# Kernel tuning notes

Measured on AMD Instinct MI355X. Metric: run time of the kernel, lower is better.

The kernel has to match this reference:

```python
import jax, jax.numpy as jnp
import numpy as np

SCALE = 2
KSIZE = 3
EPS = 0.2  # damping constant in 1/(grad^2 + 0.2)


def _unfold_patches(x, k):
    """x: [B, C, H, W] -> [B, C, k*k, H, W], zero-padded, row-major window order
    (matches torch.nn.functional.unfold channel ordering)."""
    B, C, H, W = x.shape
    p = k // 2
    xp = jnp.pad(x, ((0, 0), (0, 0), (p, p), (p, p)))
    return jnp.stack(
        [xp[:, :, i:i + H, j:j + W] for i in range(k) for j in range(k)], axis=2
    )


def setup_inputs() -> dict:
    key = jax.random.key(0)
    x = jax.random.normal(key, (4, 128, 128, 128), dtype=jnp.float32)
    return {"x": x}


def reference(x):
    B, C, H, W = x.shape
    k, s = KSIZE, SCALE
    k2 = k * k

    # channel-mean map [B, 1, H, W]
    mean = jnp.mean(x, axis=1, keepdims=True)

    # local gradients of the mean map: unfold(mean) - mean  -> [B, k2, H, W]
    grad = _unfold_patches(mean, k)[:, 0] - mean
    grad = 1.0 / (grad * grad + EPS)

    # nearest-neighbor upsample by s (F.interpolate default mode='nearest')
    up = jnp.repeat(jnp.repeat(grad, s, axis=2), s, axis=3)  # [B, k2, Hs, Ws]
    kernels = jax.nn.softmax(up, axis=1)

    # CARAFE content-aware reassembly (group=1):
    # output pixel (i, j) gathers the kxk neighborhood of source pixel
    # (i//s, j//s) of x and reduces it with kernels[:, :, i, j].
    patches = _unfold_patches(x, k)                 # [B, C, k2, H, W]
    Kr = kernels.reshape(B, k2, H, s, W, s)         # split upsampled grid
    out = jnp.einsum('bkhpwq,bckhw->bchpwq', Kr, patches)
    return out.reshape(B, C, H * s, W * s)
```

## Files before the change

kernel.cpp:

```cpp
#include <hip/hip_runtime.h>

#define NB 4
#define NC 128
#define NH 128
#define NW 128
#define EPSV 0.2f
#define TH 2

typedef float v2f __attribute__((ext_vector_type(2)));

__global__ __launch_bounds__(256) void mean_kernel(const float* __restrict__ x,
                                                   float* __restrict__ mean) {
    const int tid = threadIdx.x;
    const int pos = tid & 31;
    const int cg  = tid >> 5;
    const int gpos = blockIdx.x * 32 + pos;
    const int b    = gpos >> 12;
    const int pos4 = gpos & 4095;

    const float4* x4 = (const float4*)x;
    float4 acc = make_float4(0.f, 0.f, 0.f, 0.f);
    const int cbase = (b * NC + cg * 16) * (NH * NW / 4) + pos4;
    #pragma unroll
    for (int cc = 0; cc < 16; ++cc) {
        float4 v = x4[cbase + cc * (NH * NW / 4)];
        acc.x += v.x; acc.y += v.y; acc.z += v.z; acc.w += v.w;
    }

    __shared__ float4 red[256];
    red[tid] = acc;
    __syncthreads();
    if (tid < 32) {
        float4 s = red[tid];
        #pragma unroll
        for (int g = 1; g < 8; ++g) {
            float4 v = red[tid + 32 * g];
            s.x += v.x; s.y += v.y; s.z += v.z; s.w += v.w;
        }
        const float inv = 1.0f / NC;
        s.x *= inv; s.y *= inv; s.z *= inv; s.w *= inv;
        ((float4*)mean)[blockIdx.x * 32 + tid] = s;
    }
}

__global__ __launch_bounds__(256) void carafe_kernel(const float* __restrict__ x,
                                                     const float* __restrict__ mean,
                                                     float* __restrict__ out) {
    const int nx = gridDim.x;
    const int chunk = nx >> 3;
    const int bid = blockIdx.x;
    const int swz = (bid & 7) * chunk + (bid >> 3);

    const int b  = swz >> 6;
    const int h0 = (swz & 63) * TH;
    const int cq = blockIdx.y;

    __shared__ float wgt[TH][9][NW];

    const int tid = threadIdx.x;
    const float* mb = mean + (size_t)b * NH * NW;

    {
        const int r = tid >> 7;
        const int w = tid & 127;
        const int h = h0 + r;
        const float mc = mb[h * NW + w];
        float v[9];
        float vmax = -1e30f;
        #pragma unroll
        for (int ky = -1; ky <= 1; ++ky) {
            #pragma unroll
            for (int kx = -1; kx <= 1; ++kx) {
                const int hh = h + ky, ww = w + kx;
                const float mp = (hh >= 0 && hh < NH && ww >= 0 && ww < NW)
                                     ? mb[hh * NW + ww] : 0.0f;
                const float g = mp - mc;
                const float val = 1.0f / (g * g + EPSV);
                v[(ky + 1) * 3 + (kx + 1)] = val;
                vmax = fmaxf(vmax, val);
            }
        }
        float sum = 0.f;
        #pragma unroll
        for (int k = 0; k < 9; ++k) { v[k] = __expf(v[k] - vmax); sum += v[k]; }
        const float rs = 1.0f / sum;
        #pragma unroll
        for (int k = 0; k < 9; ++k) wgt[r][k][w] = v[k] * rs;
    }
    __syncthreads();

    const int w     = tid & (NW - 1);
    const int chalf = tid >> 7;

    float wk0[9], wk1[9];
    #pragma unroll
    for (int k = 0; k < 9; ++k) { wk0[k] = wgt[0][k][w]; wk1[k] = wgt[1][k][w]; }

    const bool hm = (h0 > 0);
    const bool hp = (h0 + TH < NH);
    const bool wm = (w > 0), wp = (w < NW - 1);

    for (int it = 0; it < 16; ++it) {
        const int c = cq * 32 + it * 2 + chalf;
        const float* xb = x + ((size_t)(b * NC + c)) * (NH * NW);

        float a[4][3];
        #pragma unroll
        for (int rr = 0; rr < 4; ++rr) {
            const int hh = h0 - 1 + rr;
            const bool hv = (rr == 0) ? hm : ((rr == 3) ? hp : true);
            const float* row = xb + hh * NW;
            a[rr][0] = (hv && wm) ? row[w - 1] : 0.f;
            a[rr][1] = hv ? row[w] : 0.f;
            a[rr][2] = (hv && wp) ? row[w + 1] : 0.f;
        }

        float v0 = 0.f, v1 = 0.f;
        #pragma unroll
        for (int ky = 0; ky < 3; ++ky) {
            #pragma unroll
            for (int kx = 0; kx < 3; ++kx) {
                v0 += wk0[ky * 3 + kx] * a[ky][kx];
                v1 += wk1[ky * 3 + kx] * a[ky + 1][kx];
            }
        }

        float* outc = out + ((size_t)(b * NC + c)) * (NH * 2) * (NW * 2);
        float* r0 = outc + (size_t)(2 * h0) * (NW * 2) + 2 * w;
        const v2f p0 = {v0, v0};
        const v2f p1 = {v1, v1};
        __builtin_nontemporal_store(p0, (v2f*)(r0));
        __builtin_nontemporal_store(p0, (v2f*)(r0 + (NW * 2)));
        __builtin_nontemporal_store(p1, (v2f*)(r0 + 2 * (NW * 2)));
        __builtin_nontemporal_store(p1, (v2f*)(r0 + 3 * (NW * 2)));
    }
}

extern "C" void kernel_launch(void* const* d_in, const int* in_sizes, int n_in,
                              void* d_out, int out_size, void* d_ws, size_t ws_size,
                              hipStream_t stream) {
    const float* x = (const float*)d_in[0];
    float* out = (float*)d_out;
    float* mean = (float*)d_ws;

    mean_kernel<<<dim3(512), dim3(256), 0, stream>>>(x, mean);
    carafe_kernel<<<dim3(NB * NH / TH, 4), dim3(256), 0, stream>>>(x, mean, out);
}
```

Baseline: 39.57 us.

## Fuse channel-mean into CARAFE kernel and widen per-thread output to float4

Removes the separate mean kernel: each block recomputes the channel mean for its two rows plus halo rows directly from x into shared memory, then builds the softmax weights and does the reassembly in one launch. The grid drops the channel-quarter dimension and uses 512-thread blocks, each thread handling 16 channels and two adjacent output columns so it emits 16-byte stores. This saves a launch and the mean round trip through memory, but each block now redundantly reads 4 rows across all 128 channels. Block count also falls to 256, which may limit latency hiding.

```diff
diff --git a/kernel.cpp b/kernel.cpp
--- a/kernel.cpp
+++ b/kernel.cpp
@@ -7,76 +7,51 @@
 #define EPSV 0.2f
 #define TH 2
 
-typedef float v2f __attribute__((ext_vector_type(2)));
+typedef float v4f __attribute__((ext_vector_type(4)));
 
-__global__ __launch_bounds__(256) void mean_kernel(const float* __restrict__ x,
-                                                   float* __restrict__ mean) {
-    const int tid = threadIdx.x;
-    const int pos = tid & 31;
-    const int cg  = tid >> 5;
-    const int gpos = blockIdx.x * 32 + pos;
-    const int b    = gpos >> 12;
-    const int pos4 = gpos & 4095;
-
-    const float4* x4 = (const float4*)x;
-    float4 acc = make_float4(0.f, 0.f, 0.f, 0.f);
-    const int cbase = (b * NC + cg * 16) * (NH * NW / 4) + pos4;
-    #pragma unroll
-    for (int cc = 0; cc < 16; ++cc) {
-        float4 v = x4[cbase + cc * (NH * NW / 4)];
-        acc.x += v.x; acc.y += v.y; acc.z += v.z; acc.w += v.w;
-    }
-
-    __shared__ float4 red[256];
-    red[tid] = acc;
-    __syncthreads();
-    if (tid < 32) {
-        float4 s = red[tid];
-        #pragma unroll
-        for (int g = 1; g < 8; ++g) {
-            float4 v = red[tid + 32 * g];
-            s.x += v.x; s.y += v.y; s.z += v.z; s.w += v.w;
-        }
-        const float inv = 1.0f / NC;
-        s.x *= inv; s.y *= inv; s.z *= inv; s.w *= inv;
-        ((float4*)mean)[blockIdx.x * 32 + tid] = s;
-    }
-}
-
-__global__ __launch_bounds__(256) void carafe_kernel(const float* __restrict__ x,
-                                                     const float* __restrict__ mean,
-                                                     float* __restrict__ out) {
-    const int nx = gridDim.x;
-    const int chunk = nx >> 3;
+__global__ __launch_bounds__(512) void fused_carafe(const float* __restrict__ x,
+                                                    float* __restrict__ out) {
+    const int chunk = gridDim.x >> 3;
     const int bid = blockIdx.x;
     const int swz = (bid & 7) * chunk + (bid >> 3);
-
     const int b  = swz >> 6;
     const int h0 = (swz & 63) * TH;
-    const int cq = blockIdx.y;
 
+    __shared__ float mrow[4][NW];
     __shared__ float wgt[TH][9][NW];
 
     const int tid = threadIdx.x;
-    const float* mb = mean + (size_t)b * NH * NW;
 
     {
         const int r = tid >> 7;
         const int w = tid & 127;
-        const int h = h0 + r;
-        const float mc = mb[h * NW + w];
+        const int hh = h0 - 1 + r;
+        float s = 0.f;
+        if (hh >= 0 && hh < NH) {
+            const float* px = x + ((size_t)b * NC * NH + hh) * NW + w;
+            #pragma unroll 16
+            for (int c = 0; c < NC; ++c)
+                s += px[(size_t)c * NH * NW];
+        }
+        mrow[r][w] = s * (1.0f / NC);
+    }
+    __syncthreads();
+
+    if (tid < 256) {
+        const int r = tid >> 7;
+        const int w = tid & 127;
+        const float mc = mrow[r + 1][w];
         float v[9];
         float vmax = -1e30f;
         #pragma unroll
-        for (int ky = -1; ky <= 1; ++ky) {
+        for (int ky = 0; ky < 3; ++ky) {
             #pragma unroll
             for (int kx = -1; kx <= 1; ++kx) {
-                const int hh = h + ky, ww = w + kx;
-                const float mp = (hh >= 0 && hh < NH && ww >= 0 && ww < NW)
-                                     ? mb[hh * NW + ww] : 0.0f;
+                const int ww = w + kx;
+                const float mp = (ww >= 0 && ww < NW) ? mrow[r + ky][ww] : 0.f;
                 const float g = mp - mc;
                 const float val = 1.0f / (g * g + EPSV);
-                v[(ky + 1) * 3 + (kx + 1)] = val;
+                v[ky * 3 + kx + 1] = val;
                 vmax = fmaxf(vmax, val);
             }
         }
@@ -89,50 +64,57 @@
     }
     __syncthreads();
 
-    const int w     = tid & (NW - 1);
-    const int chalf = tid >> 7;
+    const int wp = tid & 63;
+    const int cg = tid >> 6;
+    const int wa = 2 * wp;
 
-    float wk0[9], wk1[9];
+    float wA0[9], wB0[9], wA1[9], wB1[9];
     #pragma unroll
-    for (int k = 0; k < 9; ++k) { wk0[k] = wgt[0][k][w]; wk1[k] = wgt[1][k][w]; }
+    for (int k = 0; k < 9; ++k) {
+        wA0[k] = wgt[0][k][wa];  wB0[k] = wgt[0][k][wa + 1];
+        wA1[k] = wgt[1][k][wa];  wB1[k] = wgt[1][k][wa + 1];
+    }
 
-    const bool hm = (h0 > 0);
-    const bool hp = (h0 + TH < NH);
-    const bool wm = (w > 0), wp = (w < NW - 1);
+    const bool rv0 = (h0 > 0), rv3 = (h0 + 2 < NH);
+    const bool tv0 = (wp > 0), tv3 = (wp < 63);
 
-    for (int it = 0; it < 16; ++it) {
-        const int c = cq * 32 + it * 2 + chalf;
-        const float* xb = x + ((size_t)(b * NC + c)) * (NH * NW);
+    #pragma unroll 2
+    for (int i = 0; i < 16; ++i) {
+        const int c = cg * 16 + i;
+        const float* xc = x + ((size_t)(b * NC + c)) * (NH * NW);
 
-        float a[4][3];
+        float a[4][4];
         #pragma unroll
         for (int rr = 0; rr < 4; ++rr) {
             const int hh = h0 - 1 + rr;
-            const bool hv = (rr == 0) ? hm : ((rr == 3) ? hp : true);
-            const float* row = xb + hh * NW;
-            a[rr][0] = (hv && wm) ? row[w - 1] : 0.f;
-            a[rr][1] = hv ? row[w] : 0.f;
-            a[rr][2] = (hv && wp) ? row[w + 1] : 0.f;
+            const bool rv = (rr == 0) ? rv0 : ((rr == 3) ? rv3 : true);
+            const float* row = xc + hh * NW + wa;
+            a[rr][0] = (rv && tv0) ? row[-1] : 0.f;
+            a[rr][1] = rv ? row[0] : 0.f;
+            a[rr][2] = rv ? row[1] : 0.f;
+            a[rr][3] = (rv && tv3) ? row[2] : 0.f;
         }
 
-        float v0 = 0.f, v1 = 0.f;
+        float v0a = 0.f, v0b = 0.f, v1a = 0.f, v1b = 0.f;
         #pragma unroll
         for (int ky = 0; ky < 3; ++ky) {
             #pragma unroll
             for (int kx = 0; kx < 3; ++kx) {
-                v0 += wk0[ky * 3 + kx] * a[ky][kx];
-                v1 += wk1[ky * 3 + kx] * a[ky + 1][kx];
+                const int k = ky * 3 + kx;
+                v0a += wA0[k] * a[ky][kx];
+                v0b += wB0[k] * a[ky][kx + 1];
+                v1a += wA1[k] * a[ky + 1][kx];
+                v1b += wB1[k] * a[ky + 1][kx + 1];
             }
         }
 
-        float* outc = out + ((size_t)(b * NC + c)) * (NH * 2) * (NW * 2);
-        float* r0 = outc + (size_t)(2 * h0) * (NW * 2) + 2 * w;
-        const v2f p0 = {v0, v0};
-        const v2f p1 = {v1, v1};
-        __builtin_nontemporal_store(p0, (v2f*)(r0));
-        __builtin_nontemporal_store(p0, (v2f*)(r0 + (NW * 2)));
-        __builtin_nontemporal_store(p1, (v2f*)(r0 + 2 * (NW * 2)));
-        __builtin_nontemporal_store(p1, (v2f*)(r0 + 3 * (NW * 2)));
+        float* o = out + ((size_t)(b * NC + c) * (NH * 2) + 2 * h0) * (NW * 2) + 4 * wp;
+        const v4f p0 = {v0a, v0a, v0b, v0b};
+        const v4f p1 = {v1a, v1a, v1b, v1b};
+        __builtin_nontemporal_store(p0, (v4f*)(o));
+        __builtin_nontemporal_store(p0, (v4f*)(o + (NW * 2)));
+        __builtin_nontemporal_store(p1, (v4f*)(o + 2 * (NW * 2)));
+        __builtin_nontemporal_store(p1, (v4f*)(o + 3 * (NW * 2)));
     }
 }
 
@@ -141,8 +123,5 @@
                               hipStream_t stream) {
     const float* x = (const float*)d_in[0];
     float* out = (float*)d_out;
-    float* mean = (float*)d_ws;
-
-    mean_kernel<<<dim3(512), dim3(256), 0, stream>>>(x, mean);
-    carafe_kernel<<<dim3(NB * NH / TH, 4), dim3(256), 0, stream>>>(x, mean, out);
+    fused_carafe<<<dim3(NB * NH / TH), dim3(512), 0, stream>>>(x, out);
 }
```

After: 33.95 us. -14.2%, faster.
